# Performance work log

Hardware: AMD Instinct MI355X
Metric: run time of the kernel (lower is better)

Reference implementation:

```python
import jax, jax.numpy as jnp
import numpy as np

B, N, D, NE, NB = 512, 128, 64, 6, 4

def setup_inputs() -> dict:
    key = jax.random.key(0)
    ks = jax.random.split(key, 24)
    inp = {}
    inp['atom_types'] = jax.random.randint(ks[0], (B, N), 0, NE, dtype=jnp.int32)
    inp['positions'] = jax.random.normal(ks[1], (B, N, 3), dtype=jnp.float32)
    inp['bonds'] = jax.random.randint(ks[2], (B, N, N), 0, 5, dtype=jnp.int32)
    s = 0.05
    inp['emb'] = jax.random.normal(ks[3], (NE, D), dtype=jnp.float32)
    inp['ae_w'] = jax.random.normal(ks[4], (D,), dtype=jnp.float32) * s
    inp['ae_b'] = jax.random.normal(ks[5], (), dtype=jnp.float32) * s
    inp['ent_w'] = jax.random.normal(ks[6], (D,), dtype=jnp.float32) * s
    inp['ent_b'] = jax.random.normal(ks[7], (), dtype=jnp.float32) * s
    inp['bW'] = jax.random.normal(ks[8], (NB, D, D), dtype=jnp.float32) * s
    inp['bb'] = jax.random.normal(ks[9], (NB,), dtype=jnp.float32) * s
    H = N * D
    inp['sW1'] = jax.random.normal(ks[10], (H, 256), dtype=jnp.float32) * s
    inp['sb1'] = jnp.zeros((256,), jnp.float32)
    inp['sW2'] = jax.random.normal(ks[11], (256, 128), dtype=jnp.float32) * s
    inp['sb2'] = jnp.zeros((128,), jnp.float32)
    inp['sW3'] = jax.random.normal(ks[12], (128, 1), dtype=jnp.float32) * s
    inp['sb3'] = jnp.zeros((1,), jnp.float32)
    inp['dW1'] = jax.random.normal(ks[13], (H, 256), dtype=jnp.float32) * s
    inp['db1'] = jnp.zeros((256,), jnp.float32)
    inp['dW2'] = jax.random.normal(ks[14], (256, 128), dtype=jnp.float32) * s
    inp['db2'] = jnp.zeros((128,), jnp.float32)
    inp['dW3'] = jax.random.normal(ks[15], (128, 1), dtype=jnp.float32) * s
    inp['db3'] = jnp.zeros((1,), jnp.float32)
    return inp

def _mlp(x, W1, b1, W2, b2, W3, b3):
    h = jax.nn.relu(x @ W1 + b1)
    h = jax.nn.relu(h @ W2 + b2)
    return jax.nn.sigmoid((h @ W3 + b3)[..., 0])

def reference(atom_types, positions, bonds, emb, ae_w, ae_b, ent_w, ent_b, bW, bb,
              sW1, sb1, sW2, sb2, sW3, sb3, dW1, db1, dW2, db2, dW3, db3):
    x = emb[atom_types]                                    # [B,N,D]
    atomic_e = jnp.einsum('bnd,d->bn', x, ae_w) + ae_b     # atomic_energy linear
    atomic_s = jnp.einsum('bnd,d->bn', x, ent_w) + ent_b   # atomic_entropy linear

    # Pairwise bilinear bond energies: e[b,i,j,k] = x_i^T W_k x_j + bb_k
    t = jnp.einsum('bid,kde->bike', x, bW)                 # [B,N,K,D]
    e_all = jnp.einsum('bike,bje->bijk', t, x) + bb        # [B,N,N,K]
    bt = bonds - 1                                         # bond type index
    upper = jnp.triu(jnp.ones((N, N), dtype=bool), k=1)    # i < j
    bond_mask = upper[None] & (bonds > 0) & (bt < NB)
    e_sel = jnp.take_along_axis(e_all, jnp.clip(bt, 0, NB - 1)[..., None].astype(jnp.int32), axis=-1)[..., 0]
    bond_e = jnp.sum(jnp.where(bond_mask, e_sel, 0.0), axis=(1, 2))

    # Lennard-Jones style vdW over all i<j pairs
    diff = positions[:, :, None, :] - positions[:, None, :, :]   # [B,N,N,3]
    dist = jnp.sqrt(jnp.sum(diff * diff, axis=-1))
    vmask = upper[None] & (dist > 0)
    inv = 1.0 / jnp.where(dist > 0, dist, 1.0)
    vdw = 4.0 * (inv ** 12 - inv ** 6) * 0.1
    vdw_e = jnp.sum(jnp.where(vmask, vdw, 0.0), axis=(1, 2))

    energy = atomic_e.sum(axis=1) + bond_e + vdw_e

    # entropy: unbiased variance over atoms, summed over xyz
    pos_var = jnp.var(positions, axis=1, ddof=1).sum(axis=-1)
    entropy = atomic_s.sum(axis=1) + jnp.log(1.0 + pos_var)

    mol = x.reshape(x.shape[0], -1)                        # [B, N*D]
    stability = _mlp(mol, sW1, sb1, sW2, sb2, sW3, sb3)
    druglikeness = _mlp(mol, dW1, db1, dW2, db2, dW3, db3)
    return (energy, entropy, stability, druglikeness, x)
```

## Files before the change

### kernel.cpp

```cpp
#include <hip/hip_runtime.h>
#include <math.h>

#define BB_ 512
#define NN_ 128
#define DD_ 64
#define NE_ 6
#define NB_ 4

#define WS_PAIRE 0
#define WS_AE    144
#define WS_ENT   152
#define U16BASE_ 256
#define TDOFF_   (768 * 256)
#define W2OFF_   (1536 * 256)

typedef unsigned short u16x8 __attribute__((ext_vector_type(8)));

__device__ __forceinline__ ushort f2b(float f) {
  unsigned u = __float_as_uint(f);
  u += 0x7FFFu + ((u >> 16) & 1u);
  return (ushort)(u >> 16);
}
__device__ __forceinline__ float b2f(ushort h) {
  return __uint_as_float(((unsigned)h) << 16);
}

__device__ __forceinline__ float block_reduce256(float v, volatile float* red4,
                                                 int tid) {
#pragma unroll
  for (int off = 32; off > 0; off >>= 1) v += __shfl_down(v, off);
  __syncthreads();
  if ((tid & 63) == 0) red4[tid >> 6] = v;
  __syncthreads();
  return red4[0] + red4[1] + red4[2] + red4[3];
}

__global__ __launch_bounds__(256, 4) void k_pre(
    const float* __restrict__ emb, const float* __restrict__ ae_w,
    const float* __restrict__ ae_b, const float* __restrict__ ent_w,
    const float* __restrict__ ent_b, const float* __restrict__ bW,
    const float* __restrict__ sW1, const float* __restrict__ dW1,
    const float* __restrict__ sW2, const float* __restrict__ dW2,
    float* __restrict__ ws, float* __restrict__ out) {
  int blk = blockIdx.x;
  int tid = threadIdx.x;
  ushort* U = (ushort*)(ws + U16BASE_);

  if (blk < 512) {
    int n = blk >> 2;
    int which = (blk >> 1) & 1;
    int ohalf = blk & 1;
    const float* W1 = which ? dW1 : sW1;
    ushort* T = U + (which ? TDOFF_ : 0);
    __shared__ float e_s[NE_ * DD_];
    __shared__ float part[NE_][128];
    for (int i = tid; i < NE_ * DD_; i += 256) e_s[i] = emb[i];
    __syncthreads();
    int o_local = tid & 127;
    int dhalf = tid >> 7;
    int o = ohalf * 128 + o_local;
    float acc[NE_] = {0.f, 0.f, 0.f, 0.f, 0.f, 0.f};
    const float* Wp = W1 + ((size_t)(n * DD_ + dhalf * 32)) * 256 + o;
#pragma unroll 8
    for (int d = 0; d < 32; ++d) {
      float w = Wp[(size_t)d * 256];
#pragma unroll
      for (int t = 0; t < NE_; ++t) acc[t] += e_s[t * DD_ + dhalf * 32 + d] * w;
    }
    if (dhalf == 1) {
#pragma unroll
      for (int t = 0; t < NE_; ++t) part[t][o_local] = acc[t];
    }
    __syncthreads();
    if (dhalf == 0) {
#pragma unroll
      for (int t = 0; t < NE_; ++t)
        T[(n * NE_ + t) * 256 + o] = f2b(acc[t] + part[t][o_local]);
    }
  } else if (blk == 512) {
    float4 z = make_float4(0.f, 0.f, 0.f, 0.f);
    ((float4*)out)[tid] = z;
  } else if (blk < 657) {
    int e = blk - 513;
    int k = e / 36;
    int rem = e - k * 36;
    int ti = rem / 6, tj = rem - (rem / 6) * 6;
    int d = tid & 63;
    int qd = tid >> 6;
    const float* Wrow = bW + ((size_t)k * DD_ + d) * DD_ + qd * 16;
    const float* xj = emb + tj * DD_ + qd * 16;
    float a = 0.f;
#pragma unroll
    for (int u = 0; u < 16; ++u) a += Wrow[u] * xj[u];
    float c = emb[ti * DD_ + d] * a;
    __shared__ float red4[4];
    c = block_reduce256(c, red4, tid);
    if (tid == 0) ws[WS_PAIRE + e] = c;
  } else if (blk == 657) {
    int g = tid >> 6, lane = tid & 63;
    for (int idx = g; idx < 12; idx += 4) {
      int t = idx - (idx >= 6 ? 6 : 0);
      bool ent = idx >= 6;
      float c = emb[t * DD_ + lane] * (ent ? ent_w[lane] : ae_w[lane]);
#pragma unroll
      for (int off = 32; off > 0; off >>= 1) c += __shfl_down(c, off);
      if (lane == 0)
        ws[(ent ? WS_ENT : WS_AE) + t] = c + (ent ? ent_b[0] : ae_b[0]);
    }
  } else {
    int base = (blk - 658) * 4096 + tid;
#pragma unroll
    for (int u = 0; u < 16; ++u) {
      int e = base + u * 256;
      int head = e >> 15;
      int idx = e & 32767;
      const float* src = head ? dW2 : sW2;
      U[W2OFF_ + e] = f2b(src[idx]);
    }
  }
}

__global__ __launch_bounds__(256, 4) void k_main(
    const int* __restrict__ atom_types, const float* __restrict__ pos,
    const int* __restrict__ bonds, const float* __restrict__ emb,
    const float* __restrict__ bb, const float* __restrict__ sb1,
    const float* __restrict__ sb2, const float* __restrict__ sW3,
    const float* __restrict__ sb3, const float* __restrict__ db1,
    const float* __restrict__ db2, const float* __restrict__ dW3,
    const float* __restrict__ db3, const float* __restrict__ ws,
    float* __restrict__ out) {
  int id = blockIdx.x;
  int tid = threadIdx.x;
  const ushort* U = (const ushort*)(ws + U16BASE_);
  __shared__ float smem[3216];
  volatile float* red4 = smem + 3208;

  if (id < 256) {
    int which = id & 1;
    int mbase = (id >> 1) * 4;
    unsigned char* tyb = (unsigned char*)(smem + 3072);
    float* part = smem;
    float* h1 = smem + 2048;
    float* h2 = smem + 1024;

    for (int u = tid; u < 4 * NN_; u += 256)
      tyb[u] = (unsigned char)atom_types[(size_t)mbase * NN_ + u];
    __syncthreads();

    {
      int mi = tid >> 6;
      int half = (tid >> 5) & 1;
      int ot = tid & 31;
      const ushort* Tb = U + (which ? TDOFF_ : 0) + ot * 8;
      const unsigned char* ty = tyb + mi * NN_ + half * 64;
      float a[8] = {0.f, 0.f, 0.f, 0.f, 0.f, 0.f, 0.f, 0.f};
      for (int n0 = 0; n0 < 64; n0 += 8) {
        u16x8 v[8];
#pragma unroll
        for (int u = 0; u < 8; ++u) {
          int n = half * 64 + n0 + u;
          v[u] = *(const u16x8*)(Tb + (((n * 6) + (int)ty[n0 + u]) << 8));
        }
#pragma unroll
        for (int u = 0; u < 8; ++u) {
#pragma unroll
          for (int j = 0; j < 8; ++j) a[j] += b2f(v[u][j]);
        }
      }
      float* pp = part + mi * 512 + half * 256 + ot * 8;
#pragma unroll
      for (int j = 0; j < 8; ++j) pp[j] = a[j];
    }
    __syncthreads();
    {
      float b1v = (which ? db1 : sb1)[tid];
#pragma unroll
      for (int mm = 0; mm < 4; ++mm)
        h1[mm * 256 + tid] =
            fmaxf(part[mm * 512 + tid] + part[mm * 512 + 256 + tid] + b1v, 0.f);
    }
    __syncthreads();

    {
      int k = tid & 127;
      int kh = tid >> 7;
      const ushort* Wp = U + W2OFF_ + which * 32768 + kh * 128 * 128 + k;
      float acc[4] = {0.f, 0.f, 0.f, 0.f};
      for (int o0 = 0; o0 < 128; o0 += 16) {
        float wf[16];
#pragma unroll
        for (int u = 0; u < 16; ++u) wf[u] = b2f(Wp[(o0 + u) << 7]);
#pragma unroll
        for (int mm = 0; mm < 4; ++mm) {
          const float* hp = h1 + mm * 256 + kh * 128 + o0;
          float s = 0.f;
#pragma unroll
          for (int u = 0; u < 16; ++u) s += hp[u] * wf[u];
          acc[mm] += s;
        }
      }
      __syncthreads();
      float* scr = part;
#pragma unroll
      for (int mm = 0; mm < 4; ++mm) scr[kh * 512 + mm * 128 + k] = acc[mm];
      __syncthreads();
      if (tid < 128) {
        float b2v = (which ? db2 : sb2)[tid];
#pragma unroll
        for (int mm = 0; mm < 4; ++mm)
          h2[mm * 128 + tid] = fmaxf(
              b2v + scr[mm * 128 + tid] + scr[512 + mm * 128 + tid], 0.f);
      }
      __syncthreads();
    }

    {
      int mm = tid >> 5;
      int ln = tid & 31;
      if (mm < 4) {
        const float* W3 = which ? dW3 : sW3;
        float s = 0.f;
#pragma unroll
        for (int u = 0; u < 4; ++u) {
          int kk = ln + (u << 5);
          s += h2[mm * 128 + kk] * W3[kk];
        }
#pragma unroll
        for (int off = 16; off > 0; off >>= 1) s += __shfl_down(s, off, 32);
        if (ln == 0) {
          float b3 = (which ? db3 : sb3)[0];
          out[(2 + which) * BB_ + mbase + mm] = 1.f / (1.f + __expf(-(s + b3)));
        }
      }
    }
  } else if (id < 768) {
    int m = id - 256;
    float* pE = smem;
    float* bbv = smem + 144;
    unsigned char* tyb = (unsigned char*)(smem + 160);

    if (tid < 32) {
      int4 t4 = ((const int4*)(atom_types + (size_t)m * NN_))[tid];
      uchar4 u4;
      u4.x = (unsigned char)t4.x;
      u4.y = (unsigned char)t4.y;
      u4.z = (unsigned char)t4.z;
      u4.w = (unsigned char)t4.w;
      ((uchar4*)tyb)[tid] = u4;
    }
    if (tid >= 64 && tid < 208) pE[tid - 64] = ws[WS_PAIRE + tid - 64];
    if (tid >= 224 && tid < 228) bbv[tid - 224] = bb[tid - 224];
    __syncthreads();

    const int4* b4 = (const int4*)(bonds + (size_t)m * NN_ * NN_);
    float bp = 0.f;
#pragma unroll 4
    for (int it = 0; it < 16; ++it) {
      int li = tid + (it << 8);
      int i = li >> 5;
      int c = li & 31;
      if (c * 4 + 3 > i) {
        int4 v = b4[li];
        int j0 = c << 2;
        int ti6 = tyb[i] * 6;
        if (j0 + 0 > i && v.x > 0)
          bp += pE[(v.x - 1) * 36 + ti6 + tyb[j0 + 0]] + bbv[v.x - 1];
        if (j0 + 1 > i && v.y > 0)
          bp += pE[(v.y - 1) * 36 + ti6 + tyb[j0 + 1]] + bbv[v.y - 1];
        if (j0 + 2 > i && v.z > 0)
          bp += pE[(v.z - 1) * 36 + ti6 + tyb[j0 + 2]] + bbv[v.z - 1];
        if (j0 + 3 > i && v.w > 0)
          bp += pE[(v.w - 1) * 36 + ti6 + tyb[j0 + 3]] + bbv[v.w - 1];
      }
    }
    float e = block_reduce256(bp, red4, tid);
    if (tid == 0) atomicAdd(&out[m], e);
  } else if (id < 1280) {
    int m = id - 768;
    float4* p4 = (float4*)smem;
    float* aev = smem + 520;
    float* entv = smem + 528;
    float* redm = smem + 544;
    if (tid < 128) {
      const float* pm = pos + (size_t)m * NN_ * 3 + 3 * tid;
      p4[tid] = make_float4(pm[0], pm[1], pm[2], 0.f);
    }
    if (tid >= 128 && tid < 128 + NE_) aev[tid - 128] = ws[WS_AE + tid - 128];
    if (tid >= 160 && tid < 160 + NE_) entv[tid - 160] = ws[WS_ENT + tid - 160];
    __syncthreads();

    int i = tid >> 1;
    int half = tid & 1;
    float4 pi = p4[i];
    float vp = 0.f;
#pragma unroll 8
    for (int u = 0; u < 64; ++u) {
      int j = (half << 6) + u;
      float4 pj = p4[j];
      float dx = pi.x - pj.x;
      float dy = pi.y - pj.y;
      float dz = pi.z - pj.z;
      float d2 = dx * dx + dy * dy + dz * dz;
      if (j > i && d2 > 0.f) {
        float rc = __builtin_amdgcn_rcpf(d2);
        float r6 = rc * rc * rc;
        vp += 0.4f * (r6 * r6 - r6);
      }
    }

    float x = 0.f, y = 0.f, z = 0.f, sq = 0.f, ae = 0.f, en = 0.f;
    if (tid < 128) {
      float4 p = p4[tid];
      x = p.x;
      y = p.y;
      z = p.z;
      sq = x * x + y * y + z * z;
      int t = atom_types[(size_t)m * NN_ + tid];
      ae = aev[t];
      en = entv[t];
    }
    float vals[7] = {vp, x, y, z, sq, ae, en};
#pragma unroll
    for (int v = 0; v < 7; ++v) {
#pragma unroll
      for (int off = 32; off > 0; off >>= 1)
        vals[v] += __shfl_down(vals[v], off);
    }
    int wv = tid >> 6, ln = tid & 63;
    if (ln == 0) {
#pragma unroll
      for (int v = 0; v < 7; ++v) redm[wv * 8 + v] = vals[v];
    }
    __syncthreads();
    if (tid == 0) {
      float S[7];
#pragma unroll
      for (int v = 0; v < 7; ++v)
        S[v] = redm[v] + redm[8 + v] + redm[16 + v] + redm[24 + v];
      float var = (S[4] - (S[1] * S[1] + S[2] * S[2] + S[3] * S[3]) *
                              (1.f / NN_)) *
                  (1.f / (NN_ - 1));
      atomicAdd(&out[m], S[0] + S[5]);
      out[BB_ + m] = S[6] + logf(1.f + var);
    }
  } else {
    int m = id - 1280;
    float* e_s = smem;
    unsigned char* tyb = (unsigned char*)(smem + 384);
    for (int i = tid; i < NE_ * DD_; i += 256) e_s[i] = emb[i];
    if (tid < 32) {
      int4 t4 = ((const int4*)(atom_types + (size_t)m * NN_))[tid];
      uchar4 u4;
      u4.x = (unsigned char)t4.x;
      u4.y = (unsigned char)t4.y;
      u4.z = (unsigned char)t4.z;
      u4.w = (unsigned char)t4.w;
      ((uchar4*)tyb)[tid] = u4;
    }
    __syncthreads();
    float4* out4 = (float4*)(out + 2048 + (size_t)m * (NN_ * DD_));
#pragma unroll
    for (int u = 0; u < 8; ++u) {
      int li = tid + (u << 8);
      int n = li >> 4;
      int d0 = (li & 15) << 2;
      out4[li] = *(const float4*)&e_s[tyb[n] * DD_ + d0];
    }
  }
}

extern "C" void kernel_launch(void* const* d_in, const int* in_sizes, int n_in,
                              void* d_out, int out_size, void* d_ws,
                              size_t ws_size, hipStream_t stream) {
  const int* atom_types = (const int*)d_in[0];
  const float* positions = (const float*)d_in[1];
  const int* bonds = (const int*)d_in[2];
  const float* emb = (const float*)d_in[3];
  const float* ae_w = (const float*)d_in[4];
  const float* ae_b = (const float*)d_in[5];
  const float* ent_w = (const float*)d_in[6];
  const float* ent_b = (const float*)d_in[7];
  const float* bW = (const float*)d_in[8];
  const float* bb = (const float*)d_in[9];
  const float* sW1 = (const float*)d_in[10];
  const float* sb1 = (const float*)d_in[11];
  const float* sW2 = (const float*)d_in[12];
  const float* sb2 = (const float*)d_in[13];
  const float* sW3 = (const float*)d_in[14];
  const float* sb3 = (const float*)d_in[15];
  const float* dW1 = (const float*)d_in[16];
  const float* db1 = (const float*)d_in[17];
  const float* dW2 = (const float*)d_in[18];
  const float* db2 = (const float*)d_in[19];
  const float* dW3 = (const float*)d_in[20];
  const float* db3 = (const float*)d_in[21];
  float* out = (float*)d_out;
  float* ws = (float*)d_ws;

  hipLaunchKernelGGL(k_pre, dim3(674), dim3(256), 0, stream, emb, ae_w, ae_b,
                     ent_w, ent_b, bW, sW1, dW1, sW2, dW2, ws, out);
  hipLaunchKernelGGL(k_main, dim3(1792), dim3(256), 0, stream, atom_types,
                     positions, bonds, emb, bb, sb1, sb2, sW3, sb3, db1, db2,
                     dW3, db3, ws, out);
}
```

Baseline: 27.85 us.

## Rebalance work across two kernels: move independent stages into precompute kernel

Moves the embedding-gather output and the vdW/entropy/atomic reductions, which do not depend on precomputed tables, into the first kernel, interleaved with the W1 table blocks. The second kernel now runs only the bond energy and the MLP heads. The MLP blocks handle 2 molecules instead of 4 to double their parallelism, and they are interleaved with the bond blocks. Energy now goes through a workspace partial, which removes the output zeroing and atomics. The trade-off is less weight reuse per MLP block and more MLP blocks.

```diff
diff --git a/kernel.cpp b/kernel.cpp
--- a/kernel.cpp
+++ b/kernel.cpp
@@ -8,9 +8,8 @@
 #define NB_ 4
 
 #define WS_PAIRE 0
-#define WS_AE    144
-#define WS_ENT   152
-#define U16BASE_ 256
+#define WS_E1    160
+#define U16BASE_ 1024
 #define TDOFF_   (768 * 256)
 #define W2OFF_   (1536 * 256)
 
@@ -35,53 +34,163 @@
   return red4[0] + red4[1] + red4[2] + red4[3];
 }
 
-__global__ __launch_bounds__(256, 4) void k_pre(
+__global__ __launch_bounds__(256, 4) void k_a(
     const float* __restrict__ emb, const float* __restrict__ ae_w,
     const float* __restrict__ ae_b, const float* __restrict__ ent_w,
     const float* __restrict__ ent_b, const float* __restrict__ bW,
     const float* __restrict__ sW1, const float* __restrict__ dW1,
     const float* __restrict__ sW2, const float* __restrict__ dW2,
+    const int* __restrict__ atom_types, const float* __restrict__ pos,
     float* __restrict__ ws, float* __restrict__ out) {
-  int blk = blockIdx.x;
+  int id = blockIdx.x;
   int tid = threadIdx.x;
   ushort* U = (ushort*)(ws + U16BASE_);
-
-  if (blk < 512) {
-    int n = blk >> 2;
-    int which = (blk >> 1) & 1;
-    int ohalf = blk & 1;
-    const float* W1 = which ? dW1 : sW1;
-    ushort* T = U + (which ? TDOFF_ : 0);
-    __shared__ float e_s[NE_ * DD_];
-    __shared__ float part[NE_][128];
-    for (int i = tid; i < NE_ * DD_; i += 256) e_s[i] = emb[i];
-    __syncthreads();
-    int o_local = tid & 127;
-    int dhalf = tid >> 7;
-    int o = ohalf * 128 + o_local;
-    float acc[NE_] = {0.f, 0.f, 0.f, 0.f, 0.f, 0.f};
-    const float* Wp = W1 + ((size_t)(n * DD_ + dhalf * 32)) * 256 + o;
+  __shared__ float smem[1160];
+  volatile float* red4 = smem + 1152;
+
+  if (id < 1536) {
+    int m = id / 3;
+    int c = id - m * 3;
+    if (c == 0) {
+      int n = m >> 2;
+      int which = (m >> 1) & 1;
+      int ohalf = m & 1;
+      const float* W1 = which ? dW1 : sW1;
+      ushort* T = U + (which ? TDOFF_ : 0);
+      float* e_s = smem;
+      float* part = smem + 384;
+      for (int i = tid; i < NE_ * DD_; i += 256) e_s[i] = emb[i];
+      __syncthreads();
+      int o_local = tid & 127;
+      int dhalf = tid >> 7;
+      int o = ohalf * 128 + o_local;
+      float acc[NE_] = {0.f, 0.f, 0.f, 0.f, 0.f, 0.f};
+      const float* Wp = W1 + ((size_t)(n * DD_ + dhalf * 32)) * 256 + o;
 #pragma unroll 8
-    for (int d = 0; d < 32; ++d) {
-      float w = Wp[(size_t)d * 256];
-#pragma unroll
-      for (int t = 0; t < NE_; ++t) acc[t] += e_s[t * DD_ + dhalf * 32 + d] * w;
-    }
-    if (dhalf == 1) {
-#pragma unroll
-      for (int t = 0; t < NE_; ++t) part[t][o_local] = acc[t];
-    }
-    __syncthreads();
-    if (dhalf == 0) {
-#pragma unroll
-      for (int t = 0; t < NE_; ++t)
-        T[(n * NE_ + t) * 256 + o] = f2b(acc[t] + part[t][o_local]);
-    }
-  } else if (blk == 512) {
-    float4 z = make_float4(0.f, 0.f, 0.f, 0.f);
-    ((float4*)out)[tid] = z;
-  } else if (blk < 657) {
-    int e = blk - 513;
+      for (int d = 0; d < 32; ++d) {
+        float w = Wp[(size_t)d * 256];
+#pragma unroll
+        for (int t = 0; t < NE_; ++t)
+          acc[t] += e_s[t * DD_ + dhalf * 32 + d] * w;
+      }
+      if (dhalf == 1) {
+#pragma unroll
+        for (int t = 0; t < NE_; ++t) part[t * 128 + o_local] = acc[t];
+      }
+      __syncthreads();
+      if (dhalf == 0) {
+#pragma unroll
+        for (int t = 0; t < NE_; ++t)
+          T[(n * NE_ + t) * 256 + o] = f2b(acc[t] + part[t * 128 + o_local]);
+      }
+    } else if (c == 1) {
+      float* e_s = smem;
+      unsigned char* tyb = (unsigned char*)(smem + 384);
+      for (int i = tid; i < NE_ * DD_; i += 256) e_s[i] = emb[i];
+      if (tid < 32) {
+        int4 t4 = ((const int4*)(atom_types + (size_t)m * NN_))[tid];
+        uchar4 u4;
+        u4.x = (unsigned char)t4.x;
+        u4.y = (unsigned char)t4.y;
+        u4.z = (unsigned char)t4.z;
+        u4.w = (unsigned char)t4.w;
+        ((uchar4*)tyb)[tid] = u4;
+      }
+      __syncthreads();
+      float4* out4 = (float4*)(out + 2048 + (size_t)m * (NN_ * DD_));
+#pragma unroll
+      for (int u = 0; u < 8; ++u) {
+        int li = tid + (u << 8);
+        int n = li >> 4;
+        int d0 = (li & 15) << 2;
+        out4[li] = *(const float4*)&e_s[tyb[n] * DD_ + d0];
+      }
+    } else {
+      float4* p4 = (float4*)smem;
+      float* aev = smem + 520;
+      float* entv = smem + 528;
+      float* redm = smem + 544;
+      if (tid < 128) {
+        const float* pm = pos + (size_t)m * NN_ * 3 + 3 * tid;
+        p4[tid] = make_float4(pm[0], pm[1], pm[2], 0.f);
+      } else if (tid < 224) {
+        int v = (tid - 128) >> 3;
+        int l8 = tid & 7;
+        int t = v - (v >= 6 ? 6 : 0);
+        const float* wv = (v >= 6) ? ent_w : ae_w;
+        const float* er = emb + t * DD_ + l8 * 8;
+        const float* wr = wv + l8 * 8;
+        float s = 0.f;
+#pragma unroll
+        for (int u = 0; u < 8; ++u) s += er[u] * wr[u];
+#pragma unroll
+        for (int off = 4; off > 0; off >>= 1) s += __shfl_down(s, off, 8);
+        if (l8 == 0) {
+          if (v < 6)
+            aev[v] = s + ae_b[0];
+          else
+            entv[v - 6] = s + ent_b[0];
+        }
+      }
+      __syncthreads();
+
+      int i = tid >> 1;
+      int half = tid & 1;
+      float4 pi = p4[i];
+      float vp = 0.f;
+#pragma unroll 8
+      for (int u = 0; u < 64; ++u) {
+        int j = (half << 6) + u;
+        float4 pj = p4[j];
+        float dx = pi.x - pj.x;
+        float dy = pi.y - pj.y;
+        float dz = pi.z - pj.z;
+        float d2 = dx * dx + dy * dy + dz * dz;
+        if (j > i && d2 > 0.f) {
+          float rc = __builtin_amdgcn_rcpf(d2);
+          float r6 = rc * rc * rc;
+          vp += 0.4f * (r6 * r6 - r6);
+        }
+      }
+
+      float x = 0.f, y = 0.f, z = 0.f, sq = 0.f, ae = 0.f, en = 0.f;
+      if (tid < 128) {
+        float4 p = p4[tid];
+        x = p.x;
+        y = p.y;
+        z = p.z;
+        sq = x * x + y * y + z * z;
+        int t = atom_types[(size_t)m * NN_ + tid];
+        ae = aev[t];
+        en = entv[t];
+      }
+      float vals[7] = {vp, x, y, z, sq, ae, en};
+#pragma unroll
+      for (int v = 0; v < 7; ++v) {
+#pragma unroll
+        for (int off = 32; off > 0; off >>= 1)
+          vals[v] += __shfl_down(vals[v], off);
+      }
+      int wv2 = tid >> 6, ln = tid & 63;
+      if (ln == 0) {
+#pragma unroll
+        for (int v = 0; v < 7; ++v) redm[wv2 * 8 + v] = vals[v];
+      }
+      __syncthreads();
+      if (tid == 0) {
+        float S[7];
+#pragma unroll
+        for (int v = 0; v < 7; ++v)
+          S[v] = redm[v] + redm[8 + v] + redm[16 + v] + redm[24 + v];
+        float var = (S[4] - (S[1] * S[1] + S[2] * S[2] + S[3] * S[3]) *
+                                (1.f / NN_)) *
+                    (1.f / (NN_ - 1));
+        ws[WS_E1 + m] = S[0] + S[5];
+        out[BB_ + m] = S[6] + logf(1.f + var);
+      }
+    }
+  } else if (id < 1680) {
+    int e = id - 1536;
     int k = e / 36;
     int rem = e - k * 36;
     int ti = rem / 6, tj = rem - (rem / 6) * 6;
@@ -93,22 +202,10 @@
 #pragma unroll
     for (int u = 0; u < 16; ++u) a += Wrow[u] * xj[u];
     float c = emb[ti * DD_ + d] * a;
-    __shared__ float red4[4];
     c = block_reduce256(c, red4, tid);
     if (tid == 0) ws[WS_PAIRE + e] = c;
-  } else if (blk == 657) {
-    int g = tid >> 6, lane = tid & 63;
-    for (int idx = g; idx < 12; idx += 4) {
-      int t = idx - (idx >= 6 ? 6 : 0);
-      bool ent = idx >= 6;
-      float c = emb[t * DD_ + lane] * (ent ? ent_w[lane] : ae_w[lane]);
-#pragma unroll
-      for (int off = 32; off > 0; off >>= 1) c += __shfl_down(c, off);
-      if (lane == 0)
-        ws[(ent ? WS_ENT : WS_AE) + t] = c + (ent ? ent_b[0] : ae_b[0]);
-    }
   } else {
-    int base = (blk - 658) * 4096 + tid;
+    int base = (id - 1680) * 4096 + tid;
 #pragma unroll
     for (int u = 0; u < 16; ++u) {
       int e = base + u * 256;
@@ -120,9 +217,8 @@
   }
 }
 
-__global__ __launch_bounds__(256, 4) void k_main(
-    const int* __restrict__ atom_types, const float* __restrict__ pos,
-    const int* __restrict__ bonds, const float* __restrict__ emb,
+__global__ __launch_bounds__(256, 4) void k_b(
+    const int* __restrict__ atom_types, const int* __restrict__ bonds,
     const float* __restrict__ bb, const float* __restrict__ sb1,
     const float* __restrict__ sb2, const float* __restrict__ sW3,
     const float* __restrict__ sb3, const float* __restrict__ db1,
@@ -132,109 +228,11 @@
   int id = blockIdx.x;
   int tid = threadIdx.x;
   const ushort* U = (const ushort*)(ws + U16BASE_);
-  __shared__ float smem[3216];
-  volatile float* red4 = smem + 3208;
-
-  if (id < 256) {
-    int which = id & 1;
-    int mbase = (id >> 1) * 4;
-    unsigned char* tyb = (unsigned char*)(smem + 3072);
-    float* part = smem;
-    float* h1 = smem + 2048;
-    float* h2 = smem + 1024;
-
-    for (int u = tid; u < 4 * NN_; u += 256)
-      tyb[u] = (unsigned char)atom_types[(size_t)mbase * NN_ + u];
-    __syncthreads();
-
-    {
-      int mi = tid >> 6;
-      int half = (tid >> 5) & 1;
-      int ot = tid & 31;
-      const ushort* Tb = U + (which ? TDOFF_ : 0) + ot * 8;
-      const unsigned char* ty = tyb + mi * NN_ + half * 64;
-      float a[8] = {0.f, 0.f, 0.f, 0.f, 0.f, 0.f, 0.f, 0.f};
-      for (int n0 = 0; n0 < 64; n0 += 8) {
-        u16x8 v[8];
-#pragma unroll
-        for (int u = 0; u < 8; ++u) {
-          int n = half * 64 + n0 + u;
-          v[u] = *(const u16x8*)(Tb + (((n * 6) + (int)ty[n0 + u]) << 8));
-        }
-#pragma unroll
-        for (int u = 0; u < 8; ++u) {
-#pragma unroll
-          for (int j = 0; j < 8; ++j) a[j] += b2f(v[u][j]);
-        }
-      }
-      float* pp = part + mi * 512 + half * 256 + ot * 8;
-#pragma unroll
-      for (int j = 0; j < 8; ++j) pp[j] = a[j];
-    }
-    __syncthreads();
-    {
-      float b1v = (which ? db1 : sb1)[tid];
-#pragma unroll
-      for (int mm = 0; mm < 4; ++mm)
-        h1[mm * 256 + tid] =
-            fmaxf(part[mm * 512 + tid] + part[mm * 512 + 256 + tid] + b1v, 0.f);
-    }
-    __syncthreads();
-
-    {
-      int k = tid & 127;
-      int kh = tid >> 7;
-      const ushort* Wp = U + W2OFF_ + which * 32768 + kh * 128 * 128 + k;
-      float acc[4] = {0.f, 0.f, 0.f, 0.f};
-      for (int o0 = 0; o0 < 128; o0 += 16) {
-        float wf[16];
-#pragma unroll
-        for (int u = 0; u < 16; ++u) wf[u] = b2f(Wp[(o0 + u) << 7]);
-#pragma unroll
-        for (int mm = 0; mm < 4; ++mm) {
-          const float* hp = h1 + mm * 256 + kh * 128 + o0;
-          float s = 0.f;
-#pragma unroll
-          for (int u = 0; u < 16; ++u) s += hp[u] * wf[u];
-          acc[mm] += s;
-        }
-      }
-      __syncthreads();
-      float* scr = part;
-#pragma unroll
-      for (int mm = 0; mm < 4; ++mm) scr[kh * 512 + mm * 128 + k] = acc[mm];
-      __syncthreads();
-      if (tid < 128) {
-        float b2v = (which ? db2 : sb2)[tid];
-#pragma unroll
-        for (int mm = 0; mm < 4; ++mm)
-          h2[mm * 128 + tid] = fmaxf(
-              b2v + scr[mm * 128 + tid] + scr[512 + mm * 128 + tid], 0.f);
-      }
-      __syncthreads();
-    }
-
-    {
-      int mm = tid >> 5;
-      int ln = tid & 31;
-      if (mm < 4) {
-        const float* W3 = which ? dW3 : sW3;
-        float s = 0.f;
-#pragma unroll
-        for (int u = 0; u < 4; ++u) {
-          int kk = ln + (u << 5);
-          s += h2[mm * 128 + kk] * W3[kk];
-        }
-#pragma unroll
-        for (int off = 16; off > 0; off >>= 1) s += __shfl_down(s, off, 32);
-        if (ln == 0) {
-          float b3 = (which ? db3 : sb3)[0];
-          out[(2 + which) * BB_ + mbase + mm] = 1.f / (1.f + __expf(-(s + b3)));
-        }
-      }
-    }
-  } else if (id < 768) {
-    int m = id - 256;
+  __shared__ float smem[2632];
+  volatile float* red4 = smem + 2624;
+
+  if ((id & 1) == 0) {
+    int m = id >> 1;
     float* pE = smem;
     float* bbv = smem + 144;
     unsigned char* tyb = (unsigned char*)(smem + 160);
@@ -274,97 +272,107 @@
       }
     }
     float e = block_reduce256(bp, red4, tid);
-    if (tid == 0) atomicAdd(&out[m], e);
-  } else if (id < 1280) {
-    int m = id - 768;
-    float4* p4 = (float4*)smem;
-    float* aev = smem + 520;
-    float* entv = smem + 528;
-    float* redm = smem + 544;
+    if (tid == 0) out[m] = e + ws[WS_E1 + m];
+  } else {
+    int mlpid = id >> 1;
+    int which = mlpid & 1;
+    int mbase = (mlpid >> 1) * 2;
+    float* part = smem;
+    float* scr = smem;
+    float* h2 = smem + 512;
+    float* h1 = smem + 2048;
+    unsigned char* tyb = (unsigned char*)(smem + 2560);
+
+    tyb[tid] = (unsigned char)atom_types[(size_t)mbase * NN_ + tid];
+    __syncthreads();
+
+    {
+      int mi = tid >> 7;
+      int q = (tid >> 5) & 3;
+      int ot = tid & 31;
+      const ushort* Tb = U + (which ? TDOFF_ : 0) + ot * 8;
+      const unsigned char* ty = tyb + mi * NN_;
+      float a[8] = {0.f, 0.f, 0.f, 0.f, 0.f, 0.f, 0.f, 0.f};
+      int nb = q * 32;
+      for (int n0 = 0; n0 < 32; n0 += 8) {
+        u16x8 v[8];
+#pragma unroll
+        for (int u = 0; u < 8; ++u) {
+          int n = nb + n0 + u;
+          v[u] = *(const u16x8*)(Tb + ((n * 6 + (int)ty[n]) << 8));
+        }
+#pragma unroll
+        for (int u = 0; u < 8; ++u) {
+#pragma unroll
+          for (int j = 0; j < 8; ++j) a[j] += b2f(v[u][j]);
+        }
+      }
+      float* pp = part + mi * 1024 + q * 256 + ot * 8;
+#pragma unroll
+      for (int j = 0; j < 8; ++j) pp[j] = a[j];
+    }
+    __syncthreads();
+    {
+#pragma unroll
+      for (int li = tid; li < 512; li += 256) {
+        int mm = li >> 8;
+        int o = li & 255;
+        float s = part[mm * 1024 + o] + part[mm * 1024 + 256 + o] +
+                  part[mm * 1024 + 512 + o] + part[mm * 1024 + 768 + o];
+        h1[li] = fmaxf(s + (which ? db1 : sb1)[o], 0.f);
+      }
+    }
+    __syncthreads();
+
+    {
+      int k = tid & 127;
+      int kh = tid >> 7;
+      const ushort* Wp = U + W2OFF_ + which * 32768 + kh * 16384 + k;
+      float acc[2] = {0.f, 0.f};
+      for (int o0 = 0; o0 < 128; o0 += 16) {
+        float wf[16];
+#pragma unroll
+        for (int u = 0; u < 16; ++u) wf[u] = b2f(Wp[(o0 + u) << 7]);
+#pragma unroll
+        for (int mm = 0; mm < 2; ++mm) {
+          const float* hp = h1 + mm * 256 + kh * 128 + o0;
+          float s = 0.f;
+#pragma unroll
+          for (int u = 0; u < 16; ++u) s += hp[u] * wf[u];
+          acc[mm] += s;
+        }
+      }
+      scr[kh * 256 + 0 * 128 + k] = acc[0];
+      scr[kh * 256 + 1 * 128 + k] = acc[1];
+    }
+    __syncthreads();
     if (tid < 128) {
-      const float* pm = pos + (size_t)m * NN_ * 3 + 3 * tid;
-      p4[tid] = make_float4(pm[0], pm[1], pm[2], 0.f);
-    }
-    if (tid >= 128 && tid < 128 + NE_) aev[tid - 128] = ws[WS_AE + tid - 128];
-    if (tid >= 160 && tid < 160 + NE_) entv[tid - 160] = ws[WS_ENT + tid - 160];
-    __syncthreads();
-
-    int i = tid >> 1;
-    int half = tid & 1;
-    float4 pi = p4[i];
-    float vp = 0.f;
-#pragma unroll 8
-    for (int u = 0; u < 64; ++u) {
-      int j = (half << 6) + u;
-      float4 pj = p4[j];
-      float dx = pi.x - pj.x;
-      float dy = pi.y - pj.y;
-      float dz = pi.z - pj.z;
-      float d2 = dx * dx + dy * dy + dz * dz;
-      if (j > i && d2 > 0.f) {
-        float rc = __builtin_amdgcn_rcpf(d2);
-        float r6 = rc * rc * rc;
-        vp += 0.4f * (r6 * r6 - r6);
-      }
-    }
-
-    float x = 0.f, y = 0.f, z = 0.f, sq = 0.f, ae = 0.f, en = 0.f;
-    if (tid < 128) {
-      float4 p = p4[tid];
-      x = p.x;
-      y = p.y;
-      z = p.z;
-      sq = x * x + y * y + z * z;
-      int t = atom_types[(size_t)m * NN_ + tid];
-      ae = aev[t];
-      en = entv[t];
-    }
-    float vals[7] = {vp, x, y, z, sq, ae, en};
-#pragma unroll
-    for (int v = 0; v < 7; ++v) {
-#pragma unroll
-      for (int off = 32; off > 0; off >>= 1)
-        vals[v] += __shfl_down(vals[v], off);
-    }
-    int wv = tid >> 6, ln = tid & 63;
-    if (ln == 0) {
-#pragma unroll
-      for (int v = 0; v < 7; ++v) redm[wv * 8 + v] = vals[v];
-    }
-    __syncthreads();
-    if (tid == 0) {
-      float S[7];
-#pragma unroll
-      for (int v = 0; v < 7; ++v)
-        S[v] = redm[v] + redm[8 + v] + redm[16 + v] + redm[24 + v];
-      float var = (S[4] - (S[1] * S[1] + S[2] * S[2] + S[3] * S[3]) *
-                              (1.f / NN_)) *
-                  (1.f / (NN_ - 1));
-      atomicAdd(&out[m], S[0] + S[5]);
-      out[BB_ + m] = S[6] + logf(1.f + var);
-    }
-  } else {
-    int m = id - 1280;
-    float* e_s = smem;
-    unsigned char* tyb = (unsigned char*)(smem + 384);
-    for (int i = tid; i < NE_ * DD_; i += 256) e_s[i] = emb[i];
-    if (tid < 32) {
-      int4 t4 = ((const int4*)(atom_types + (size_t)m * NN_))[tid];
-      uchar4 u4;
-      u4.x = (unsigned char)t4.x;
-      u4.y = (unsigned char)t4.y;
-      u4.z = (unsigned char)t4.z;
-      u4.w = (unsigned char)t4.w;
-      ((uchar4*)tyb)[tid] = u4;
-    }
-    __syncthreads();
-    float4* out4 = (float4*)(out + 2048 + (size_t)m * (NN_ * DD_));
-#pragma unroll
-    for (int u = 0; u < 8; ++u) {
-      int li = tid + (u << 8);
-      int n = li >> 4;
-      int d0 = (li & 15) << 2;
-      out4[li] = *(const float4*)&e_s[tyb[n] * DD_ + d0];
+      float b2v = (which ? db2 : sb2)[tid];
+#pragma unroll
+      for (int mm = 0; mm < 2; ++mm)
+        h2[mm * 128 + tid] =
+            fmaxf(b2v + scr[mm * 128 + tid] + scr[256 + mm * 128 + tid], 0.f);
+    }
+    __syncthreads();
+
+    {
+      int mm = tid >> 5;
+      int ln = tid & 31;
+      if (mm < 2) {
+        const float* W3 = which ? dW3 : sW3;
+        float s = 0.f;
+#pragma unroll
+        for (int u = 0; u < 4; ++u) {
+          int kk = ln + (u << 5);
+          s += h2[mm * 128 + kk] * W3[kk];
+        }
+#pragma unroll
+        for (int off = 16; off > 0; off >>= 1) s += __shfl_down(s, off, 32);
+        if (ln == 0) {
+          float b3 = (which ? db3 : sb3)[0];
+          out[(2 + which) * BB_ + mbase + mm] = 1.f / (1.f + __expf(-(s + b3)));
+        }
+      }
     }
   }
 }
@@ -397,9 +405,9 @@
   float* out = (float*)d_out;
   float* ws = (float*)d_ws;
 
-  hipLaunchKernelGGL(k_pre, dim3(674), dim3(256), 0, stream, emb, ae_w, ae_b,
-                     ent_w, ent_b, bW, sW1, dW1, sW2, dW2, ws, out);
-  hipLaunchKernelGGL(k_main, dim3(1792), dim3(256), 0, stream, atom_types,
-                     positions, bonds, emb, bb, sb1, sb2, sW3, sb3, db1, db2,
-                     dW3, db3, ws, out);
-}
+  hipLaunchKernelGGL(k_a, dim3(1696), dim3(256), 0, stream, emb, ae_w, ae_b,
+                     ent_w, ent_b, bW, sW1, dW1, sW2, dW2, atom_types,
+                     positions, ws, out);
+  hipLaunchKernelGGL(k_b, dim3(1024), dim3(256), 0, stream, atom_types, bonds,
+                     bb, sb1, sb2, sW3, sb3, db1, db2, dW3, db3, ws, out);
+}
```

Measured after the change: 28.08 us. Within noise of the previous version (+0.8%).

## Split W1 precompute finer, transpose W2 for vector loads, interleave main-kernel block roles

Applied to the files above, without the earlier changes.

The W1 embedding-projection precompute now uses twice as many blocks, each splitting the reduction over four d-quarters, which gives the pre-kernel more parallelism. W2 is stored transposed in bf16 so the MLP layer-2 loop can read weights with 16-byte vector loads instead of strided scalar loads. The main kernel's block roles (MLP, bond, vdW, embedding output) are interleaved in a 1:2:2:2 pattern, so heavy and light work are spread evenly across CUs rather than grouped by role. In exchange, the transposed W2 conversion reads the source with a strided pattern, and the finer split adds a shared-memory reduction step.

```diff
diff --git a/kernel.cpp b/kernel.cpp
--- a/kernel.cpp
+++ b/kernel.cpp
@@ -46,42 +46,43 @@
   int tid = threadIdx.x;
   ushort* U = (ushort*)(ws + U16BASE_);
 
-  if (blk < 512) {
-    int n = blk >> 2;
-    int which = (blk >> 1) & 1;
-    int ohalf = blk & 1;
+  if (blk < 1024) {
+    int n = blk >> 3;
+    int sub = blk & 7;
+    int which = sub >> 2;
+    int oquad = sub & 3;
     const float* W1 = which ? dW1 : sW1;
     ushort* T = U + (which ? TDOFF_ : 0);
     __shared__ float e_s[NE_ * DD_];
-    __shared__ float part[NE_][128];
+    __shared__ float part[4][NE_][64];
     for (int i = tid; i < NE_ * DD_; i += 256) e_s[i] = emb[i];
     __syncthreads();
-    int o_local = tid & 127;
-    int dhalf = tid >> 7;
-    int o = ohalf * 128 + o_local;
+    int dquad = tid >> 6;
+    int o_local = tid & 63;
+    int o = oquad * 64 + o_local;
     float acc[NE_] = {0.f, 0.f, 0.f, 0.f, 0.f, 0.f};
-    const float* Wp = W1 + ((size_t)(n * DD_ + dhalf * 32)) * 256 + o;
-#pragma unroll 8
-    for (int d = 0; d < 32; ++d) {
+    const float* Wp = W1 + ((size_t)(n * DD_ + dquad * 16)) * 256 + o;
+#pragma unroll
+    for (int d = 0; d < 16; ++d) {
       float w = Wp[(size_t)d * 256];
 #pragma unroll
-      for (int t = 0; t < NE_; ++t) acc[t] += e_s[t * DD_ + dhalf * 32 + d] * w;
-    }
-    if (dhalf == 1) {
-#pragma unroll
-      for (int t = 0; t < NE_; ++t) part[t][o_local] = acc[t];
-    }
-    __syncthreads();
-    if (dhalf == 0) {
-#pragma unroll
-      for (int t = 0; t < NE_; ++t)
-        T[(n * NE_ + t) * 256 + o] = f2b(acc[t] + part[t][o_local]);
-    }
-  } else if (blk == 512) {
+      for (int t = 0; t < NE_; ++t) acc[t] += e_s[t * DD_ + dquad * 16 + d] * w;
+    }
+#pragma unroll
+    for (int t = 0; t < NE_; ++t) part[dquad][t][o_local] = acc[t];
+    __syncthreads();
+    if (tid < NE_ * 64) {
+      int t = tid >> 6;
+      int ol = tid & 63;
+      float s = part[0][t][ol] + part[1][t][ol] + part[2][t][ol] +
+                part[3][t][ol];
+      T[(n * NE_ + t) * 256 + oquad * 64 + ol] = f2b(s);
+    }
+  } else if (blk == 1024) {
     float4 z = make_float4(0.f, 0.f, 0.f, 0.f);
     ((float4*)out)[tid] = z;
-  } else if (blk < 657) {
-    int e = blk - 513;
+  } else if (blk < 1169) {
+    int e = blk - 1025;
     int k = e / 36;
     int rem = e - k * 36;
     int ti = rem / 6, tj = rem - (rem / 6) * 6;
@@ -96,7 +97,7 @@
     __shared__ float red4[4];
     c = block_reduce256(c, red4, tid);
     if (tid == 0) ws[WS_PAIRE + e] = c;
-  } else if (blk == 657) {
+  } else if (blk == 1169) {
     int g = tid >> 6, lane = tid & 63;
     for (int idx = g; idx < 12; idx += 4) {
       int t = idx - (idx >= 6 ? 6 : 0);
@@ -108,14 +109,16 @@
         ws[(ent ? WS_ENT : WS_AE) + t] = c + (ent ? ent_b[0] : ae_b[0]);
     }
   } else {
-    int base = (blk - 658) * 4096 + tid;
+    int base = (blk - 1170) * 4096 + tid;
 #pragma unroll
     for (int u = 0; u < 16; ++u) {
       int e = base + u * 256;
       int head = e >> 15;
       int idx = e & 32767;
+      int k = idx >> 8;
+      int o = idx & 255;
       const float* src = head ? dW2 : sW2;
-      U[W2OFF_ + e] = f2b(src[idx]);
+      U[W2OFF_ + head * 32768 + idx] = f2b(src[o * 128 + k]);
     }
   }
 }
@@ -130,14 +133,16 @@
     const float* __restrict__ db3, const float* __restrict__ ws,
     float* __restrict__ out) {
   int id = blockIdx.x;
+  int j = id / 7;
+  int g = id - j * 7;
   int tid = threadIdx.x;
   const ushort* U = (const ushort*)(ws + U16BASE_);
   __shared__ float smem[3216];
   volatile float* red4 = smem + 3208;
 
-  if (id < 256) {
-    int which = id & 1;
-    int mbase = (id >> 1) * 4;
+  if (g == 0) {
+    int which = j & 1;
+    int mbase = (j >> 1) * 4;
     unsigned char* tyb = (unsigned char*)(smem + 3072);
     float* part = smem;
     float* h1 = smem + 2048;
@@ -164,12 +169,12 @@
 #pragma unroll
         for (int u = 0; u < 8; ++u) {
 #pragma unroll
-          for (int j = 0; j < 8; ++j) a[j] += b2f(v[u][j]);
+          for (int jj = 0; jj < 8; ++jj) a[jj] += b2f(v[u][jj]);
         }
       }
       float* pp = part + mi * 512 + half * 256 + ot * 8;
 #pragma unroll
-      for (int j = 0; j < 8; ++j) pp[j] = a[j];
+      for (int jj = 0; jj < 8; ++jj) pp[jj] = a[jj];
     }
     __syncthreads();
     {
@@ -184,12 +189,17 @@
     {
       int k = tid & 127;
       int kh = tid >> 7;
-      const ushort* Wp = U + W2OFF_ + which * 32768 + kh * 128 * 128 + k;
+      const ushort* Wp = U + W2OFF_ + which * 32768 + k * 256 + kh * 128;
       float acc[4] = {0.f, 0.f, 0.f, 0.f};
       for (int o0 = 0; o0 < 128; o0 += 16) {
+        u16x8 wa = *(const u16x8*)(Wp + o0);
+        u16x8 wb = *(const u16x8*)(Wp + o0 + 8);
         float wf[16];
 #pragma unroll
-        for (int u = 0; u < 16; ++u) wf[u] = b2f(Wp[(o0 + u) << 7]);
+        for (int u = 0; u < 8; ++u) {
+          wf[u] = b2f(wa[u]);
+          wf[u + 8] = b2f(wb[u]);
+        }
 #pragma unroll
         for (int mm = 0; mm < 4; ++mm) {
           const float* hp = h1 + mm * 256 + kh * 128 + o0;
@@ -233,8 +243,8 @@
         }
       }
     }
-  } else if (id < 768) {
-    int m = id - 256;
+  } else if (g < 3) {
+    int m = j * 2 + (g - 1);
     float* pE = smem;
     float* bbv = smem + 144;
     unsigned char* tyb = (unsigned char*)(smem + 160);
@@ -275,8 +285,8 @@
     }
     float e = block_reduce256(bp, red4, tid);
     if (tid == 0) atomicAdd(&out[m], e);
-  } else if (id < 1280) {
-    int m = id - 768;
+  } else if (g < 5) {
+    int m = j * 2 + (g - 3);
     float4* p4 = (float4*)smem;
     float* aev = smem + 520;
     float* entv = smem + 528;
@@ -295,13 +305,13 @@
     float vp = 0.f;
 #pragma unroll 8
     for (int u = 0; u < 64; ++u) {
-      int j = (half << 6) + u;
-      float4 pj = p4[j];
+      int jj = (half << 6) + u;
+      float4 pj = p4[jj];
       float dx = pi.x - pj.x;
       float dy = pi.y - pj.y;
       float dz = pi.z - pj.z;
       float d2 = dx * dx + dy * dy + dz * dz;
-      if (j > i && d2 > 0.f) {
+      if (jj > i && d2 > 0.f) {
         float rc = __builtin_amdgcn_rcpf(d2);
         float r6 = rc * rc * rc;
         vp += 0.4f * (r6 * r6 - r6);
@@ -344,7 +354,7 @@
       out[BB_ + m] = S[6] + logf(1.f + var);
     }
   } else {
-    int m = id - 1280;
+    int m = j * 2 + (g - 5);
     float* e_s = smem;
     unsigned char* tyb = (unsigned char*)(smem + 384);
     for (int i = tid; i < NE_ * DD_; i += 256) e_s[i] = emb[i];
@@ -397,7 +407,7 @@
   float* out = (float*)d_out;
   float* ws = (float*)d_ws;
 
-  hipLaunchKernelGGL(k_pre, dim3(674), dim3(256), 0, stream, emb, ae_w, ae_b,
+  hipLaunchKernelGGL(k_pre, dim3(1186), dim3(256), 0, stream, emb, ae_w, ae_b,
                      ent_w, ent_b, bW, sW1, dW1, sW2, dW2, ws, out);
   hipLaunchKernelGGL(k_main, dim3(1792), dim3(256), 0, stream, atom_types,
                      positions, bonds, emb, bb, sb1, sb2, sW3, sb3, db1, db2,
```

After: 34.07 us. 1.22x slower.
